# Kernel optimization log

Measured on AMD Instinct MI355X. Metric: run time of the kernel, lower is better.

## Reference

```python
import jax, jax.numpy as jnp
import numpy as np

N, H, G = 500_000, 128, 50_000


def setup_inputs() -> dict:
    key = jax.random.key(0)
    k1, k2, k3, k4, k5, k6, k7 = jax.random.split(key, 7)
    x_src = jax.random.normal(k1, (N, H), dtype=jnp.float32)
    imputed_embs = jax.random.normal(k2, (G, H), dtype=jnp.float32)
    src_ids = jnp.sort(jax.random.randint(k3, (N,), 0, G, dtype=jnp.int32))
    s = 1.0 / np.sqrt(2 * H)
    W1 = jax.random.uniform(k4, (H, 2 * H), jnp.float32, -s, s)  # cat_linear1
    b1 = jax.random.uniform(k5, (H,), jnp.float32, -s, s)
    W2 = jax.random.uniform(k6, (H, 2 * H), jnp.float32, -s, s)  # cat_linear2
    b2 = jax.random.uniform(k7, (H,), jnp.float32, -s, s)
    return {"x_src": x_src, "imputed_embs": imputed_embs, "W1": W1, "b1": b1,
            "W2": W2, "b2": b2, "src_ids": src_ids}


def reference(x_src, imputed_embs, W1, b1, W2, b2, src_ids):
    n, h = x_src.shape
    g = imputed_embs.shape[0]
    # group index per row: boundaries where adjacent sorted src_ids differ
    boundary = jnp.concatenate([jnp.zeros((1,), jnp.int32),
                                (src_ids[1:] != src_ids[:-1]).astype(jnp.int32)])
    gid = jnp.cumsum(boundary)  # [N] group id (0..num_groups-1)
    # segment mean of x_src per group (parallel replacement of the python loop)
    seg_sum = jax.ops.segment_sum(x_src, gid, num_segments=g)
    counts = jax.ops.segment_sum(jnp.ones((n,), x_src.dtype), gid, num_segments=g)
    seg_mean = seg_sum / jnp.maximum(counts, 1.0)[:, None]
    # original loop never writes the mean for the LAST group (or unused rows):
    written = (jnp.arange(g) < gid[-1])[:, None]
    imp_second = jnp.where(written, seg_mean, imputed_embs)
    # x_out rows: [x_src_i, imputed_embs[group(i)]]
    x_cat = jnp.concatenate([x_src, imputed_embs[gid]], axis=1)      # [N, 2H]
    imp_cat = jnp.concatenate([imputed_embs, imp_second], axis=1)    # [G, 2H]
    x_out = x_cat @ W1.T + b1
    imputed_out = imp_cat @ W2.T + b2
    return (x_out, imputed_out)
```

## Files before the change

kernel.cpp:

```cpp
#include <hip/hip_runtime.h>

typedef __attribute__((ext_vector_type(8))) short short8;
typedef __attribute__((ext_vector_type(4))) float f32x4;

static __device__ __forceinline__ unsigned short f2bf(float f) {
    union { float f; unsigned int u; } v; v.f = f;
    unsigned int r = v.u + 0x7fffu + ((v.u >> 16) & 1u);
    return (unsigned short)(r >> 16);
}

static __device__ __forceinline__ short8 pack8(float4 a, float4 b) {
    short8 r;
    r[0] = (short)f2bf(a.x); r[1] = (short)f2bf(a.y);
    r[2] = (short)f2bf(a.z); r[3] = (short)f2bf(a.w);
    r[4] = (short)f2bf(b.x); r[5] = (short)f2bf(b.y);
    r[6] = (short)f2bf(b.z); r[7] = (short)f2bf(b.w);
    return r;
}

static __device__ __forceinline__ void dma16(const void* g, void* l) {
    __builtin_amdgcn_global_load_lds(
        (const __attribute__((address_space(1))) unsigned int*)g,
        (__attribute__((address_space(3))) unsigned int*)l, 16, 0, 0);
}

static __device__ __forceinline__ float4 lds_rd16(const float* buf, int boff, int sw) {
    return *(const float4*)((const char*)buf + (boff ^ sw));
}

__global__ void k_zero(uint4* p, int n16) {
    int i = blockIdx.x * blockDim.x + threadIdx.x;
    if (i < n16) p[i] = uint4{0u, 0u, 0u, 0u};
}

__global__ void k_convw(const float* __restrict__ W1, const float* __restrict__ W2,
                        unsigned short* W1af, unsigned short* W1bf,
                        unsigned short* W2af, unsigned short* W2bf) {
    int T = blockIdx.x * 256 + threadIdx.x;
    int mat = T >> 11;
    int rem = T & 2047;
    int f = rem >> 6, lane = rem & 63;
    int wc = f >> 4, t = (f >> 2) & 3, kk = f & 3;
    int p = lane & 15, q = lane >> 4;
    int row = wc * 64 + t * 16 + p;
    int col = (mat & 1) * 128 + kk * 32 + q * 8;
    const float* src = (mat < 2 ? W1 : W2) + row * 256 + col;
    unsigned short* dst = (mat == 0 ? W1af : mat == 1 ? W1bf : mat == 2 ? W2af : W2bf);
    short8 v;
#pragma unroll
    for (int j = 0; j < 8; ++j) v[j] = (short)f2bf(src[j]);
    *(short8*)&dst[(size_t)f * 512 + lane * 8] = v;
}

__global__ void k_mark(const int* __restrict__ ids, int* __restrict__ cum, int n) {
    int i = blockIdx.x * blockDim.x + threadIdx.x;
    if (i < n) cum[ids[i]] = 1;
}

__global__ __launch_bounds__(256) void k_scan1(int* __restrict__ cum, int* __restrict__ bsum, int G) {
    __shared__ int ws[4];
    int tid = threadIdx.x;
    int base = blockIdx.x * 1024 + tid * 4;
    int a0 = 0, a1 = 0, a2 = 0, a3 = 0;
    if (base + 0 < G) a0 = cum[base + 0];
    if (base + 1 < G) a1 = cum[base + 1];
    if (base + 2 < G) a2 = cum[base + 2];
    if (base + 3 < G) a3 = cum[base + 3];
    int s = a0 + a1 + a2 + a3;
    int lane = tid & 63;
    int v = s;
#pragma unroll
    for (int off = 1; off < 64; off <<= 1) {
        int u = __shfl_up(v, off, 64);
        if (lane >= off) v += u;
    }
    if (lane == 63) ws[tid >> 6] = v;
    __syncthreads();
    int wof = 0;
    for (int w = 0; w < (tid >> 6); ++w) wof += ws[w];
    int excl = wof + v - s;
    int r0 = excl + a0, r1 = r0 + a1, r2 = r1 + a2, r3 = r2 + a3;
    if (base + 0 < G) cum[base + 0] = r0;
    if (base + 1 < G) cum[base + 1] = r1;
    if (base + 2 < G) cum[base + 2] = r2;
    if (base + 3 < G) cum[base + 3] = r3;
    if (tid == 255) bsum[blockIdx.x] = excl + s;
}

__global__ void k_scan2(int* __restrict__ bsum, int nb) {
    int t = threadIdx.x;
    int v = (t < nb) ? bsum[t] : 0;
#pragma unroll
    for (int off = 1; off < 64; off <<= 1) {
        int u = __shfl_up(v, off, 64);
        if (t >= off) v += u;
    }
    if (t < nb) bsum[t] = v;
}

__global__ void k_gid(const int* __restrict__ ids, const int* __restrict__ cum,
                      const int* __restrict__ bsum, int* __restrict__ gid,
                      int* __restrict__ gstart, int* __restrict__ ngr, int n) {
    int i = blockIdx.x * blockDim.x + threadIdx.x;
    if (i >= n) return;
    int v = ids[i];
    int blk = v >> 10;
    int g = cum[v] + (blk ? bsum[blk - 1] : 0) - 1;
    gid[i] = g;
    if (i == 0 || ids[i - 1] != v) gstart[g] = i;
    if (i == n - 1) { gstart[g + 1] = n; *ngr = g + 1; }
}

__global__ __launch_bounds__(256) void k_gsum(
    const float* __restrict__ x, const float* __restrict__ emb,
    const int* __restrict__ gstart, const int* __restrict__ ngr,
    unsigned short* __restrict__ imps, int G) {
    int w = blockIdx.x * 4 + (threadIdx.x >> 6);
    int lane = threadIdx.x & 63;
    if (w >= G) return;
    int ng = *ngr;
    float2 m;
    if (w < ng - 1) {
        int a = gstart[w], b = gstart[w + 1];
        int n = b - a;
        const float* px = x + (size_t)a * 128 + lane * 2;
        float2 c0, c1, c2, c3, n0, n1, n2, n3;
        c0 = *(const float2*)(px);
        c1 = *(const float2*)(px + (size_t)min(1, n - 1) * 128);
        c2 = *(const float2*)(px + (size_t)min(2, n - 1) * 128);
        c3 = *(const float2*)(px + (size_t)min(3, n - 1) * 128);
        float sx = 0.f, sy = 0.f;
        for (int base = 0; base < n; base += 4) {
            if (base + 4 < n) {
                n0 = *(const float2*)(px + (size_t)(base + 4) * 128);
                n1 = *(const float2*)(px + (size_t)min(base + 5, n - 1) * 128);
                n2 = *(const float2*)(px + (size_t)min(base + 6, n - 1) * 128);
                n3 = *(const float2*)(px + (size_t)min(base + 7, n - 1) * 128);
            }
            sx += c0.x; sy += c0.y;
            if (base + 1 < n) { sx += c1.x; sy += c1.y; }
            if (base + 2 < n) { sx += c2.x; sy += c2.y; }
            if (base + 3 < n) { sx += c3.x; sy += c3.y; }
            c0 = n0; c1 = n1; c2 = n2; c3 = n3;
        }
        float inv = 1.0f / (float)n;
        m.x = sx * inv; m.y = sy * inv;
    } else {
        m = *(const float2*)(emb + (size_t)w * 128 + lane * 2);
    }
    unsigned int pk = (unsigned int)f2bf(m.x) | ((unsigned int)f2bf(m.y) << 16);
    ((unsigned int*)imps)[(size_t)w * 64 + lane] = pk;
}

__global__ __launch_bounds__(256, 2) void k_egemm(
    const float* __restrict__ emb, const unsigned short* __restrict__ Wf,
    const float* __restrict__ b1, float* __restrict__ E1, int G) {
    __shared__ __align__(16) float ebuf[16384];
    int tid = threadIdx.x, lane = tid & 63, wid = tid >> 6;
    int p = lane & 15, q = lane >> 4;
    int wr = wid >> 1, wc = wid & 1;
    int row0 = blockIdx.x * 128;

    short8 bfr[4][4];
#pragma unroll
    for (int t = 0; t < 4; ++t)
#pragma unroll
        for (int kk = 0; kk < 4; ++kk)
            bfr[t][kk] = *(const short8*)&Wf[(size_t)((wc * 4 + t) * 4 + kk) * 512 + lane * 8];
    float b1v[4];
#pragma unroll
    for (int t = 0; t < 4; ++t) b1v[t] = b1[wc * 64 + t * 16 + p];

    long long maxb = (long long)G * 512 - 16;
#pragma unroll
    for (int k = 0; k < 16; ++k) {
        int doff = k * 4096 + tid * 16;
        int r = doff >> 9;
        long long s = (long long)(row0 + r) * 512 + (long long)((doff & 511) ^ ((r & 7) << 4));
        s = s < maxb ? s : maxb;
        dma16((const char*)emb + s, (char*)ebuf + doff);
    }
    asm volatile("s_waitcnt vmcnt(0)" ::: "memory");
    __builtin_amdgcn_s_barrier();
    __builtin_amdgcn_sched_barrier(0);

    int sw = (p & 7) << 4;
#pragma unroll
    for (int tt = 0; tt < 4; ++tt) {
        int lr = wr * 64 + tt * 16 + p;
        short8 afr[4];
#pragma unroll
        for (int kk = 0; kk < 4; ++kk) {
            int boff = lr * 512 + kk * 128 + q * 32;
            float4 v0 = lds_rd16(ebuf, boff, sw);
            float4 v1 = lds_rd16(ebuf, boff + 16, sw);
            afr[kk] = pack8(v0, v1);
        }
        f32x4 acc[4];
#pragma unroll
        for (int t = 0; t < 4; ++t) acc[t] = f32x4{0.f, 0.f, 0.f, 0.f};
#pragma unroll
        for (int t = 0; t < 4; ++t)
#pragma unroll
            for (int kk = 0; kk < 4; ++kk)
                acc[t] = __builtin_amdgcn_mfma_f32_16x16x32_bf16(afr[kk], bfr[t][kk], acc[t], 0, 0, 0);
#pragma unroll
        for (int t = 0; t < 4; ++t) {
            int colb = wc * 64 + t * 16 + p;
#pragma unroll
            for (int rg = 0; rg < 4; ++rg) {
                int rr = row0 + wr * 64 + tt * 16 + q * 4 + rg;
                if (rr < G) E1[(size_t)rr * 128 + colb] = acc[t][rg] + b1v[t];
            }
        }
    }
}

__global__ __launch_bounds__(256, 2) void k_xgemm(
    const float* __restrict__ x, const unsigned short* __restrict__ Wf,
    const int* __restrict__ gid, const float* __restrict__ E1,
    float* __restrict__ out, int N, int nwg) {
    __shared__ __align__(16) float xbuf[16384];
    int tid = threadIdx.x, lane = tid & 63, wid = tid >> 6;
    int p = lane & 15, q = lane >> 4;
    int wr = wid >> 1, wc = wid & 1;
    int orig = blockIdx.x;
    int qq = nwg >> 3, rr8 = nwg & 7;
    int xcd = orig & 7, idx = orig >> 3;
    int bid = (xcd < rr8 ? xcd * (qq + 1) : rr8 * (qq + 1) + (xcd - rr8) * qq) + idx;
    int row0 = bid * 128;

    short8 bfr[4][4];
#pragma unroll
    for (int t = 0; t < 4; ++t)
#pragma unroll
        for (int kk = 0; kk < 4; ++kk)
            bfr[t][kk] = *(const short8*)&Wf[(size_t)((wc * 4 + t) * 4 + kk) * 512 + lane * 8];

    int gt0 = gid[min(row0 + wr * 64 + 0 * 16 + p, N - 1)];
    int gt1 = gid[min(row0 + wr * 64 + 1 * 16 + p, N - 1)];
    int gt2 = gid[min(row0 + wr * 64 + 2 * 16 + p, N - 1)];
    int gt3 = gid[min(row0 + wr * 64 + 3 * 16 + p, N - 1)];

    long long maxb = (long long)N * 512 - 16;
#pragma unroll
    for (int k = 0; k < 16; ++k) {
        int doff = k * 4096 + tid * 16;
        int r = doff >> 9;
        long long s = (long long)(row0 + r) * 512 + (long long)((doff & 511) ^ ((r & 7) << 4));
        s = s < maxb ? s : maxb;
        dma16((const char*)x + s, (char*)xbuf + doff);
    }
    asm volatile("s_waitcnt vmcnt(0)" ::: "memory");
    __builtin_amdgcn_s_barrier();
    __builtin_amdgcn_sched_barrier(0);

    int sw = (p & 7) << 4;
#pragma unroll
    for (int tt = 0; tt < 4; ++tt) {
        int gt = (tt == 0) ? gt0 : (tt == 1) ? gt1 : (tt == 2) ? gt2 : gt3;
        int lr = wr * 64 + tt * 16 + p;
        short8 afr[4];
#pragma unroll
        for (int kk = 0; kk < 4; ++kk) {
            int boff = lr * 512 + kk * 128 + q * 32;
            float4 v0 = lds_rd16(xbuf, boff, sw);
            float4 v1 = lds_rd16(xbuf, boff + 16, sw);
            afr[kk] = pack8(v0, v1);
        }
        int g4[4];
#pragma unroll
        for (int rg = 0; rg < 4; ++rg) g4[rg] = __shfl(gt, q * 4 + rg);
        float ev[4][4];
#pragma unroll
        for (int t = 0; t < 4; ++t) {
            int colb = wc * 64 + t * 16 + p;
#pragma unroll
            for (int rg = 0; rg < 4; ++rg)
                ev[t][rg] = E1[(size_t)g4[rg] * 128 + colb];
        }
        f32x4 acc[4];
#pragma unroll
        for (int t = 0; t < 4; ++t) acc[t] = f32x4{0.f, 0.f, 0.f, 0.f};
#pragma unroll
        for (int t = 0; t < 4; ++t)
#pragma unroll
            for (int kk = 0; kk < 4; ++kk)
                acc[t] = __builtin_amdgcn_mfma_f32_16x16x32_bf16(afr[kk], bfr[t][kk], acc[t], 0, 0, 0);
#pragma unroll
        for (int t = 0; t < 4; ++t) {
            int colb = wc * 64 + t * 16 + p;
#pragma unroll
            for (int rg = 0; rg < 4; ++rg) {
                int rr = row0 + wr * 64 + tt * 16 + q * 4 + rg;
                if (rr < N) out[(size_t)rr * 128 + colb] = acc[t][rg] + ev[t][rg];
            }
        }
    }
}

__global__ __launch_bounds__(256, 2) void k_igemm(
    const float* __restrict__ emb, const unsigned short* __restrict__ imps,
    const unsigned short* __restrict__ Waf, const unsigned short* __restrict__ Wbf,
    const float* __restrict__ b2, float* __restrict__ out2, int G) {
    __shared__ __align__(16) float ebuf[8192];
    __shared__ __align__(16) unsigned short ibuf[8192];
    int tid = threadIdx.x, lane = tid & 63, wid = tid >> 6;
    int p = lane & 15, q = lane >> 4;
    int wr = wid >> 1, wc = wid & 1;
    int row0 = blockIdx.x * 64;

    short8 bfrA[4][4], bfrB[4][4];
#pragma unroll
    for (int t = 0; t < 4; ++t)
#pragma unroll
        for (int kk = 0; kk < 4; ++kk) {
            bfrA[t][kk] = *(const short8*)&Waf[(size_t)((wc * 4 + t) * 4 + kk) * 512 + lane * 8];
            bfrB[t][kk] = *(const short8*)&Wbf[(size_t)((wc * 4 + t) * 4 + kk) * 512 + lane * 8];
        }
    float b2v[4];
#pragma unroll
    for (int t = 0; t < 4; ++t) b2v[t] = b2[wc * 64 + t * 16 + p];

    long long maxe = (long long)G * 512 - 16;
    long long maxi = (long long)G * 256 - 16;
#pragma unroll
    for (int k = 0; k < 8; ++k) {
        int doff = k * 4096 + tid * 16;
        int r = doff >> 9;
        long long s = (long long)(row0 + r) * 512 + (long long)((doff & 511) ^ ((r & 7) << 4));
        s = s < maxe ? s : maxe;
        dma16((const char*)emb + s, (char*)ebuf + doff);
    }
#pragma unroll
    for (int k = 0; k < 4; ++k) {
        int doff = k * 4096 + tid * 16;
        int r = doff >> 8;
        long long s = (long long)(row0 + r) * 256 + (long long)((doff & 255) ^ ((r & 7) << 4));
        s = s < maxi ? s : maxi;
        dma16((const char*)imps + s, (char*)ibuf + doff);
    }
    asm volatile("s_waitcnt vmcnt(0)" ::: "memory");
    __builtin_amdgcn_s_barrier();
    __builtin_amdgcn_sched_barrier(0);

    int sw = (p & 7) << 4;
#pragma unroll
    for (int tt = 0; tt < 2; ++tt) {
        int lr = wr * 32 + tt * 16 + p;
        short8 ae[4], ia[4];
#pragma unroll
        for (int kk = 0; kk < 4; ++kk) {
            int boff = lr * 512 + kk * 128 + q * 32;
            float4 v0 = lds_rd16(ebuf, boff, sw);
            float4 v1 = lds_rd16(ebuf, boff + 16, sw);
            ae[kk] = pack8(v0, v1);
            int boff2 = lr * 256 + ((kk * 64 + q * 16) ^ sw);
            ia[kk] = *(const short8*)((const char*)ibuf + boff2);
        }
        f32x4 acc[4];
#pragma unroll
        for (int t = 0; t < 4; ++t) acc[t] = f32x4{0.f, 0.f, 0.f, 0.f};
#pragma unroll
        for (int kk = 0; kk < 4; ++kk)
#pragma unroll
            for (int t = 0; t < 4; ++t) {
                acc[t] = __builtin_amdgcn_mfma_f32_16x16x32_bf16(ae[kk], bfrA[t][kk], acc[t], 0, 0, 0);
                acc[t] = __builtin_amdgcn_mfma_f32_16x16x32_bf16(ia[kk], bfrB[t][kk], acc[t], 0, 0, 0);
            }
#pragma unroll
        for (int t = 0; t < 4; ++t) {
            int colb = wc * 64 + t * 16 + p;
#pragma unroll
            for (int rg = 0; rg < 4; ++rg) {
                int rr = row0 + wr * 32 + tt * 16 + q * 4 + rg;
                if (rr < G) out2[(size_t)rr * 128 + colb] = acc[t][rg] + b2v[t];
            }
        }
    }
}

extern "C" void kernel_launch(void* const* d_in, const int* in_sizes, int n_in,
                              void* d_out, int out_size, void* d_ws, size_t ws_size,
                              hipStream_t stream) {
    const float* x   = (const float*)d_in[0];
    const float* emb = (const float*)d_in[1];
    const float* W1  = (const float*)d_in[2];
    const float* b1  = (const float*)d_in[3];
    const float* W2  = (const float*)d_in[4];
    const float* b2  = (const float*)d_in[5];
    const int*   ids = (const int*)d_in[6];
    const int H = 128;
    const int N = in_sizes[6];
    const int G = in_sizes[1] / H;

    float* out  = (float*)d_out;
    float* out2 = out + (size_t)N * H;
    float* E1   = out2;

    char* ws = (char*)d_ws;
    size_t off = 0;
    int*   cum    = (int*)(ws + off);   off += (size_t)G * 4;
    size_t zbytes = off;
    off = (off + 255) & ~(size_t)255;
    int* bsum   = (int*)(ws + off); off += 64 * 4;          off = (off + 255) & ~(size_t)255;
    int* gid    = (int*)(ws + off); off += (size_t)N * 4;   off = (off + 255) & ~(size_t)255;
    int* gstart = (int*)(ws + off); off += (size_t)(G + 1) * 4; off = (off + 255) & ~(size_t)255;
    int* ngr    = (int*)(ws + off); off += 256;
    unsigned short* W1af = (unsigned short*)(ws + off); off += (size_t)H * H * 2;
    unsigned short* W1bf = (unsigned short*)(ws + off); off += (size_t)H * H * 2;
    unsigned short* W2af = (unsigned short*)(ws + off); off += (size_t)H * H * 2;
    unsigned short* W2bf = (unsigned short*)(ws + off); off += (size_t)H * H * 2;
    unsigned short* imps = (unsigned short*)(ws + off); off += (size_t)G * H * 2;

    int n16 = (int)((zbytes + 15) / 16);
    int nb = (G + 1023) >> 10;
    int nwgX = (N + 127) >> 7;
    int nwgE = (G + 127) >> 7;
    int nwgI = (G + 63) >> 6;
    k_zero<<<(n16 + 255) / 256, 256, 0, stream>>>((uint4*)ws, n16);
    k_convw<<<32, 256, 0, stream>>>(W1, W2, W1af, W1bf, W2af, W2bf);
    k_mark<<<(N + 255) / 256, 256, 0, stream>>>(ids, cum, N);
    k_scan1<<<nb, 256, 0, stream>>>(cum, bsum, G);
    k_scan2<<<1, 64, 0, stream>>>(bsum, nb);
    k_gid<<<(N + 255) / 256, 256, 0, stream>>>(ids, cum, bsum, gid, gstart, ngr, N);
    k_gsum<<<(G + 3) / 4, 256, 0, stream>>>(x, emb, gstart, ngr, imps, G);
    k_egemm<<<nwgE, 256, 0, stream>>>(emb, W1bf, b1, E1, G);
    k_xgemm<<<nwgX, 256, 0, stream>>>(x, W1af, gid, E1, out, N, nwgX);
    k_igemm<<<nwgI, 256, 0, stream>>>(emb, imps, W2af, W2bf, b2, out2, G);
}
```

Before: 227.5 us.

## Fuse segment-mean reduction into x GEMM epilogue using LDS tile

Removes the separate group-sum kernel that re-read all of x from global memory. The per-group sums are now computed in the x-GEMM epilogue from the x tile already staged in shared memory. Groups fully inside a 64-row half-tile write their bf16 mean directly. Split groups accumulate via atomics into a zeroed float buffer, which a small fix-up kernel then normalizes. This adds a larger zeroing pass, atomic traffic and a serial per-thread reduction at the end of the GEMM.

```diff
diff --git a/kernel.cpp b/kernel.cpp
--- a/kernel.cpp
+++ b/kernel.cpp
@@ -111,47 +111,6 @@
     if (i == n - 1) { gstart[g + 1] = n; *ngr = g + 1; }
 }
 
-__global__ __launch_bounds__(256) void k_gsum(
-    const float* __restrict__ x, const float* __restrict__ emb,
-    const int* __restrict__ gstart, const int* __restrict__ ngr,
-    unsigned short* __restrict__ imps, int G) {
-    int w = blockIdx.x * 4 + (threadIdx.x >> 6);
-    int lane = threadIdx.x & 63;
-    if (w >= G) return;
-    int ng = *ngr;
-    float2 m;
-    if (w < ng - 1) {
-        int a = gstart[w], b = gstart[w + 1];
-        int n = b - a;
-        const float* px = x + (size_t)a * 128 + lane * 2;
-        float2 c0, c1, c2, c3, n0, n1, n2, n3;
-        c0 = *(const float2*)(px);
-        c1 = *(const float2*)(px + (size_t)min(1, n - 1) * 128);
-        c2 = *(const float2*)(px + (size_t)min(2, n - 1) * 128);
-        c3 = *(const float2*)(px + (size_t)min(3, n - 1) * 128);
-        float sx = 0.f, sy = 0.f;
-        for (int base = 0; base < n; base += 4) {
-            if (base + 4 < n) {
-                n0 = *(const float2*)(px + (size_t)(base + 4) * 128);
-                n1 = *(const float2*)(px + (size_t)min(base + 5, n - 1) * 128);
-                n2 = *(const float2*)(px + (size_t)min(base + 6, n - 1) * 128);
-                n3 = *(const float2*)(px + (size_t)min(base + 7, n - 1) * 128);
-            }
-            sx += c0.x; sy += c0.y;
-            if (base + 1 < n) { sx += c1.x; sy += c1.y; }
-            if (base + 2 < n) { sx += c2.x; sy += c2.y; }
-            if (base + 3 < n) { sx += c3.x; sy += c3.y; }
-            c0 = n0; c1 = n1; c2 = n2; c3 = n3;
-        }
-        float inv = 1.0f / (float)n;
-        m.x = sx * inv; m.y = sy * inv;
-    } else {
-        m = *(const float2*)(emb + (size_t)w * 128 + lane * 2);
-    }
-    unsigned int pk = (unsigned int)f2bf(m.x) | ((unsigned int)f2bf(m.y) << 16);
-    ((unsigned int*)imps)[(size_t)w * 64 + lane] = pk;
-}
-
 __global__ __launch_bounds__(256, 2) void k_egemm(
     const float* __restrict__ emb, const unsigned short* __restrict__ Wf,
     const float* __restrict__ b1, float* __restrict__ E1, int G) {
@@ -219,7 +178,9 @@
 __global__ __launch_bounds__(256, 2) void k_xgemm(
     const float* __restrict__ x, const unsigned short* __restrict__ Wf,
     const int* __restrict__ gid, const float* __restrict__ E1,
-    float* __restrict__ out, int N, int nwg) {
+    const int* __restrict__ gstart, const int* __restrict__ ngr,
+    float* __restrict__ out, unsigned short* __restrict__ imps,
+    float* __restrict__ segsum, int N, int nwg) {
     __shared__ __align__(16) float xbuf[16384];
     int tid = threadIdx.x, lane = tid & 63, wid = tid >> 6;
     int p = lane & 15, q = lane >> 4;
@@ -297,6 +258,57 @@
             }
         }
     }
+
+    int c = tid & 127;
+    int h = tid >> 7;
+    int lo = row0 + h * 64;
+    if (lo < N) {
+        int hi = min(lo + 64, N);
+        int ng = *ngr;
+        int g = gid[lo];
+        int rs = gstart[g];
+        for (;;) {
+            int re = gstart[g + 1];
+            int a = rs > lo ? rs : lo;
+            int b = re < hi ? re : hi;
+            float s = 0.f;
+            for (int r = a; r < b; ++r) {
+                int lrr = r - row0;
+                s += *(const float*)((const char*)xbuf + lrr * 512 + ((c * 4) ^ ((lrr & 7) << 4)));
+            }
+            bool contained = (rs >= lo) && (re <= hi);
+            if (contained) {
+                if (g < ng - 1)
+                    imps[(size_t)g * 128 + c] = f2bf(s / (float)(re - rs));
+            } else {
+                atomicAdd(&segsum[(size_t)g * 128 + c], s);
+            }
+            if (re >= hi) break;
+            rs = re; ++g;
+        }
+    }
+}
+
+__global__ __launch_bounds__(256) void k_fix(
+    const float* __restrict__ segsum, const float* __restrict__ emb,
+    const int* __restrict__ gstart, const int* __restrict__ ngr,
+    unsigned short* __restrict__ imps, int G) {
+    int g = blockIdx.x * 4 + (threadIdx.x >> 6);
+    int lane = threadIdx.x & 63;
+    if (g >= G) return;
+    int ng = *ngr;
+    float2 m;
+    if (g < ng - 1) {
+        int a = gstart[g], b = gstart[g + 1];
+        if ((a >> 6) == ((b - 1) >> 6)) return;
+        float inv = 1.0f / (float)(b - a);
+        float2 s = *(const float2*)&segsum[(size_t)g * 128 + lane * 2];
+        m.x = s.x * inv; m.y = s.y * inv;
+    } else {
+        m = *(const float2*)&emb[(size_t)g * 128 + lane * 2];
+    }
+    unsigned int pk = (unsigned int)f2bf(m.x) | ((unsigned int)f2bf(m.y) << 16);
+    ((unsigned int*)imps)[(size_t)g * 64 + lane] = pk;
 }
 
 __global__ __launch_bounds__(256, 2) void k_igemm(
@@ -400,6 +412,7 @@
 
     char* ws = (char*)d_ws;
     size_t off = 0;
+    float* segsum = (float*)(ws + off); off += (size_t)G * H * 4;
     int*   cum    = (int*)(ws + off);   off += (size_t)G * 4;
     size_t zbytes = off;
     off = (off + 255) & ~(size_t)255;
@@ -424,8 +437,8 @@
     k_scan1<<<nb, 256, 0, stream>>>(cum, bsum, G);
     k_scan2<<<1, 64, 0, stream>>>(bsum, nb);
     k_gid<<<(N + 255) / 256, 256, 0, stream>>>(ids, cum, bsum, gid, gstart, ngr, N);
-    k_gsum<<<(G + 3) / 4, 256, 0, stream>>>(x, emb, gstart, ngr, imps, G);
     k_egemm<<<nwgE, 256, 0, stream>>>(emb, W1bf, b1, E1, G);
-    k_xgemm<<<nwgX, 256, 0, stream>>>(x, W1af, gid, E1, out, N, nwgX);
+    k_xgemm<<<nwgX, 256, 0, stream>>>(x, W1af, gid, E1, gstart, ngr, out, imps, segsum, N, nwgX);
+    k_fix<<<(G + 3) / 4, 256, 0, stream>>>(segsum, emb, gstart, ngr, imps, G);
     k_igemm<<<nwgI, 256, 0, stream>>>(emb, imps, W2af, W2bf, b2, out2, G);
 }
```

Measured after the change: 219.1 us. -3.7%, faster.
